# Performance work log

Hardware: AMD Instinct MI355X
Metric: run time of the kernel (lower is better)

## Reference

```python
import jax, jax.numpy as jnp
import numpy as np
from jax import lax

T, B = 128, 256
I, H = 512, 1024
V, O = 128, 64


def setup_inputs() -> dict:
    key = jax.random.key(0)
    ks = jax.random.split(key, 8)
    s_ih = 1.0 / np.sqrt(H)
    return {
        "input": jax.random.randint(ks[0], (T, B), 0, V, dtype=jnp.int64),
        "h0": jnp.zeros((1, B, H), jnp.float32),
        "c0": jnp.zeros((1, B, H), jnp.float32),
        "emb": jax.random.normal(ks[1], (V, I), jnp.float32),
        "w_ih": jax.random.uniform(ks[2], (4 * H, I), jnp.float32, -s_ih, s_ih),
        "w_hh": jax.random.uniform(ks[3], (4 * H, H), jnp.float32, -s_ih, s_ih),
        "b_ih": jax.random.uniform(ks[4], (4 * H,), jnp.float32, -s_ih, s_ih),
        "b_hh": jax.random.uniform(ks[5], (4 * H,), jnp.float32, -s_ih, s_ih),
        "w_out": jax.random.uniform(ks[6], (O, H), jnp.float32, -s_ih, s_ih),
        "b_out": jax.random.uniform(ks[7], (O,), jnp.float32, -s_ih, s_ih),
    }


def reference(input, h0, c0, emb, w_ih, w_hh, b_ih, b_hh, w_out, b_out):
    # Embedding lookup: [T, B] -> [T, B, I]
    x = emb[input]
    b = b_ih + b_hh  # fuse the two bias adds

    def step(carry, xt):
        h, c = carry  # [B, H] each
        gates = xt @ w_ih.T + h @ w_hh.T + b  # [B, 4H]
        i, f, g, o = jnp.split(gates, 4, axis=-1)  # torch gate order: i,f,g,o
        i = jax.nn.sigmoid(i)
        f = jax.nn.sigmoid(f)
        g = jnp.tanh(g)
        o = jax.nn.sigmoid(o)
        c_new = f * c + i * g
        h_new = o * jnp.tanh(c_new)
        return (h_new, c_new), h_new

    (h_last, _), _ = lax.scan(step, (h0[0], c0[0]), x)
    # out_layer(lstm_out[-1].unsqueeze(0))[-1] == last hidden through linear head
    return h_last @ w_out.T + b_out  # [B, O]
```

## Files before the change

kernel.cpp:

```cpp
#include <hip/hip_runtime.h>

typedef __attribute__((ext_vector_type(4)))  int int4v;
typedef __attribute__((ext_vector_type(16))) int i32x16;

union B16 { int4v v; signed char c[16]; };

__device__ __forceinline__ float rcp_(float x){ return __builtin_amdgcn_rcpf(x); }
__device__ __forceinline__ float sigm(float x){ return rcp_(1.f + __expf(-x)); }
__device__ __forceinline__ float tanh_(float x){
  float e = __expf(-2.f * fabsf(x));
  float r = (1.f - e) * rcp_(1.f + e);
  return copysignf(r, x);
}
__device__ __forceinline__ void h_limbs(float h, int& a1, int& a0){
  float f1 = floorf(h * 128.f);
  f1 = fminf(fmaxf(f1, -128.f), 127.f);
  float r = fmaf(h, 32768.f, f1 * -256.f) - 128.f;
  float f0 = fminf(rintf(r), 127.f);
  a1 = (int)f1; a0 = (int)f0;
}

__device__ __forceinline__ void issue_l128_cc(const void* p, int4v& d){
  asm volatile("global_load_dwordx4 %0, %1, off sc0 sc1" : "=&v"(d) : "v"(p) : "memory");
}

__global__ __launch_bounds__(256) void prep_kernel(
    const float* __restrict__ emb, const float* __restrict__ w_ih,
    const float* __restrict__ b_ih, const float* __restrict__ b_hh,
    const float* __restrict__ h0, float* __restrict__ G_in,
    char* __restrict__ a1buf, char* __restrict__ a0buf)
{
  __shared__ __align__(16) float wt[16 * 512];
  const int tid = threadIdx.x;
  const int colbase = blockIdx.x << 4;
  #pragma unroll
  for (int i = 0; i < 8; ++i){
    int f = tid + (i << 8);
    int r = f >> 7, q = (f & 127) << 2;
    *(float4*)&wt[(r << 9) + q] = *(const float4*)&w_ih[((size_t)(colbase + r) << 9) + q];
  }
  __syncthreads();
  const int v_ = tid & 127, ch = tid >> 7;
  float acc[8] = {0,0,0,0,0,0,0,0};
  const float* ep = emb + ((size_t)v_ << 9);
  for (int kq = 0; kq < 128; ++kq){
    float4 e = *(const float4*)(ep + (kq << 2));
    #pragma unroll
    for (int c = 0; c < 8; ++c){
      float4 w = *(const float4*)&wt[(((ch << 3) + c) << 9) + (kq << 2)];
      acc[c] += e.x * w.x + e.y * w.y + e.z * w.z + e.w * w.w;
    }
  }
  const int col0 = colbase + (ch << 3);
  #pragma unroll
  for (int c = 0; c < 8; ++c) acc[c] += b_ih[col0 + c] + b_hh[col0 + c];
  float* gp = &G_in[((size_t)v_ << 12) + col0];
  float4 r0 = {acc[0], acc[1], acc[2], acc[3]};
  float4 r1 = {acc[4], acc[5], acc[6], acc[7]};
  *(float4*)gp = r0;
  *(float4*)(gp + 4) = r1;

  int g0 = (blockIdx.x << 10) + (tid << 2);
  float4 hv = *(const float4*)&h0[g0];
  int a1x,a0x,a1y,a0y,a1z,a0z,a1w,a0w;
  h_limbs(hv.x, a1x, a0x); h_limbs(hv.y, a1y, a0y);
  h_limbs(hv.z, a1z, a0z); h_limbs(hv.w, a1w, a0w);
  unsigned u1 = (unsigned)(a1x & 255) | ((unsigned)(a1y & 255) << 8)
              | ((unsigned)(a1z & 255) << 16) | ((unsigned)(a1w & 255) << 24);
  unsigned u0 = (unsigned)(a0x & 255) | ((unsigned)(a0y & 255) << 8)
              | ((unsigned)(a0z & 255) << 16) | ((unsigned)(a0w & 255) << 24);
  ((unsigned*)a1buf)[g0 >> 2] = u1;
  ((unsigned*)a0buf)[g0 >> 2] = u0;
}

__global__ __launch_bounds__(256, 1) void lstm_kernel(
    const int* __restrict__ input, const float* __restrict__ c0,
    const float* __restrict__ w_hh, const float* __restrict__ w_out,
    const float* __restrict__ b_out, const float* __restrict__ G_in,
    char* __restrict__ a1base, char* __restrict__ a0base,
    unsigned* __restrict__ flags, float* __restrict__ out)
{
  const int tid  = threadIdx.x;
  const int lane = tid & 63;
  const int wid  = tid >> 6;
  const int bg   = blockIdx.x >> 5;
  const int cg   = blockIdx.x & 31;
  const int bl   = tid >> 3;
  const int u4   = (tid & 7) << 2;
  const int row  = tid & 31;
  const int grp  = tid >> 5;

  __shared__ __align__(16) unsigned long long sA1[4096];
  __shared__ __align__(16) unsigned long long sA0[4096];
  __shared__ __align__(16) float sG[32 * 132];
  __shared__ float sKc[128];

  int4v b1f[32], b0f[32];
  {
    const float* wrow = w_hh + (size_t)(wid * 1024 + cg * 32 + (lane & 31)) * 1024;
    const int kb0 = (lane >> 5) << 4;
    float csum = 0.f;
    #pragma unroll
    for (int ks = 0; ks < 32; ++ks){
      B16 v1, v0;
      #pragma unroll
      for (int q = 0; q < 4; ++q){
        float4 w4 = *(const float4*)&wrow[ks * 32 + kb0 + (q << 2)];
        float wa[4] = {w4.x, w4.y, w4.z, w4.w};
        #pragma unroll
        for (int j = 0; j < 4; ++j){
          float w = wa[j];
          csum += w;
          float s1 = rintf(w * 2048.f);
          float s0 = fminf(rintf(fmaf(w, 524288.f, s1 * -256.f)), 127.f);
          v1.c[(q << 2) + j] = (signed char)(int)s1;
          v0.c[(q << 2) + j] = (signed char)(int)s0;
        }
      }
      b1f[ks] = v1.v; b0f[ks] = v0.v;
    }
    csum += __shfl_xor(csum, 32, 64);
    if (lane < 32) sKc[(wid << 5) + lane] = csum * 0.00390625f;
  }

  const int b = (bg << 5) + bl;
  float4 cr = *(const float4*)&c0[((size_t)b << 10) + (cg << 5) + u4];
  unsigned* slots = &flags[bg * 32];
  unsigned* myslot = &flags[bg * 32 + cg];
  const size_t rbase = (size_t)((bg << 5) + row) << 10;

  #pragma unroll 1
  for (int t = 0; t < 128; ++t){
    const char* s1b = a1base + (size_t)(t & 1) * 262144;
    const char* s0b = a0base + (size_t)(t & 1) * 262144;
    char* d1b = a1base + (size_t)((t + 1) & 1) * 262144;
    char* d0b = a0base + (size_t)((t + 1) & 1) * 262144;
    const unsigned target = (unsigned)t;

    int iv = input[t * 256 + b];
    const float* gp = G_in + ((size_t)iv << 12) + (cg << 5) + u4;
    float4 q0 = *(const float4*)(gp);
    float4 q1 = *(const float4*)(gp + 1024);
    float4 q2 = *(const float4*)(gp + 2048);
    float4 q3 = *(const float4*)(gp + 3072);

    if (wid == 0 && target){
      int guard = 0;
      for (;;){
        unsigned v = (lane < 32)
          ? __hip_atomic_load(&slots[lane], __ATOMIC_RELAXED, __HIP_MEMORY_SCOPE_AGENT)
          : 0xFFFFFFFFu;
        if (__ballot(lane >= 16 || v >= target) == ~0ull) break;
        if (++guard > (1 << 20)) break;
      }
    }
    __syncthreads();

    int4v gv1[8], gv0[8];
    #pragma unroll
    for (int i = 0; i < 4; ++i){
      size_t off = rbase + ((size_t)(grp + (i << 3)) << 4);
      issue_l128_cc(s1b + off, gv1[i]);
      issue_l128_cc(s0b + off, gv0[i]);
    }

    if (wid == 0 && target){
      int guard = 0;
      for (;;){
        unsigned v = (lane < 32)
          ? __hip_atomic_load(&slots[lane], __ATOMIC_RELAXED, __HIP_MEMORY_SCOPE_AGENT)
          : 0xFFFFFFFFu;
        if (__ballot(v >= target) == ~0ull) break;
        if (++guard > (1 << 20)) break;
      }
    }
    __syncthreads();

    #pragma unroll
    for (int i = 4; i < 8; ++i){
      size_t off = rbase + ((size_t)(grp + (i << 3)) << 4);
      issue_l128_cc(s1b + off, gv1[i]);
      issue_l128_cc(s0b + off, gv0[i]);
    }

    i32x16 acc_hi = {}, acc_m1 = {}, acc_m2 = {};
    const int4v* A1 = (const int4v*)sA1;
    const int4v* A0 = (const int4v*)sA0;
    #pragma unroll
    for (int c = 0; c < 4; ++c){
      if      (c == 0) asm volatile("s_waitcnt vmcnt(12)" ::: "memory");
      else if (c == 1) asm volatile("s_waitcnt vmcnt(8)"  ::: "memory");
      else if (c == 2) asm volatile("s_waitcnt vmcnt(4)"  ::: "memory");
      else             asm volatile("s_waitcnt vmcnt(0)"  ::: "memory");
      __builtin_amdgcn_sched_barrier(0);
      #pragma unroll
      for (int j = 0; j < 2; ++j){
        const int i = 2*c + j;
        const int m = grp + (i << 3);
        const int lidx = ((((m >> 1) << 6) + ((m & 1) << 5) + row)) << 1;
        *(int4v*)&sA1[lidx] = gv1[i];
        *(int4v*)&sA0[lidx] = gv0[i];
      }
      asm volatile("s_waitcnt lgkmcnt(0)" ::: "memory");
      __builtin_amdgcn_sched_barrier(0);
      __builtin_amdgcn_s_barrier();
      __builtin_amdgcn_sched_barrier(0);
      #pragma unroll
      for (int ks = 8*c; ks < 8*c + 8; ++ks){
        int4v af1 = A1[(ks << 6) + lane];
        acc_hi = __builtin_amdgcn_mfma_i32_32x32x32_i8(af1, b1f[ks], acc_hi, 0, 0, 0);
        acc_m1 = __builtin_amdgcn_mfma_i32_32x32x32_i8(af1, b0f[ks], acc_m1, 0, 0, 0);
        int4v af0 = A0[(ks << 6) + lane];
        acc_m2 = __builtin_amdgcn_mfma_i32_32x32x32_i8(af0, b1f[ks], acc_m2, 0, 0, 0);
      }
    }

    {
      const int col = (wid << 5) + (lane & 31);
      const int rb  = (lane >> 5) << 2;
      #pragma unroll
      for (int r = 0; r < 16; ++r){
        int rrow = (r & 3) + ((r >> 2) << 3) + rb;
        sG[rrow * 132 + col] = 3.814697265625e-06f     * (float)acc_hi[r]
                             + 1.4901161193847656e-08f * (float)(acc_m1[r] + acc_m2[r]);
      }
    }
    __syncthreads();

    {
      float4 kI = *(const float4*)&sKc[ 0 + u4];
      float4 kF = *(const float4*)&sKc[32 + u4];
      float4 kG = *(const float4*)&sKc[64 + u4];
      float4 kO = *(const float4*)&sKc[96 + u4];
      float4 gI = *(const float4*)&sG[bl * 132 +  0 + u4];
      float4 gF = *(const float4*)&sG[bl * 132 + 32 + u4];
      float4 gG = *(const float4*)&sG[bl * 132 + 64 + u4];
      float4 gO = *(const float4*)&sG[bl * 132 + 96 + u4];
      int a1x,a0x,a1y,a0y,a1z,a0z,a1w,a0w;
      { float I=sigm(gI.x+q0.x+kI.x), F=sigm(gF.x+q1.x+kF.x), G=tanh_(gG.x+q2.x+kG.x), O=sigm(gO.x+q3.x+kO.x);
        float Cn=F*cr.x+I*G; cr.x=Cn; h_limbs(O*tanh_(Cn), a1x, a0x); }
      { float I=sigm(gI.y+q0.y+kI.y), F=sigm(gF.y+q1.y+kF.y), G=tanh_(gG.y+q2.y+kG.y), O=sigm(gO.y+q3.y+kO.y);
        float Cn=F*cr.y+I*G; cr.y=Cn; h_limbs(O*tanh_(Cn), a1y, a0y); }
      { float I=sigm(gI.z+q0.z+kI.z), F=sigm(gF.z+q1.z+kF.z), G=tanh_(gG.z+q2.z+kG.z), O=sigm(gO.z+q3.z+kO.z);
        float Cn=F*cr.z+I*G; cr.z=Cn; h_limbs(O*tanh_(Cn), a1z, a0z); }
      { float I=sigm(gI.w+q0.w+kI.w), F=sigm(gF.w+q1.w+kF.w), G=tanh_(gG.w+q2.w+kG.w), O=sigm(gO.w+q3.w+kO.w);
        float Cn=F*cr.w+I*G; cr.w=Cn; h_limbs(O*tanh_(Cn), a1w, a0w); }
      unsigned u1 = (unsigned)(a1x & 255) | ((unsigned)(a1y & 255) << 8)
                  | ((unsigned)(a1z & 255) << 16) | ((unsigned)(a1w & 255) << 24);
      unsigned u0 = (unsigned)(a0x & 255) | ((unsigned)(a0y & 255) << 8)
                  | ((unsigned)(a0z & 255) << 16) | ((unsigned)(a0w & 255) << 24);
      size_t eidx = (((size_t)b << 10) + (cg << 5) + u4) >> 2;
      __hip_atomic_store((unsigned*)d1b + eidx, u1, __ATOMIC_RELAXED, __HIP_MEMORY_SCOPE_AGENT);
      __hip_atomic_store((unsigned*)d0b + eidx, u0, __ATOMIC_RELAXED, __HIP_MEMORY_SCOPE_AGENT);
    }
    __syncthreads();
    if (tid == 0)
      __hip_atomic_store(myslot, (unsigned)(t + 1), __ATOMIC_RELAXED, __HIP_MEMORY_SCOPE_AGENT);
  }

  if (wid == 0){
    int guard = 0;
    for (;;){
      unsigned v = (lane < 32)
        ? __hip_atomic_load(&slots[lane], __ATOMIC_RELAXED, __HIP_MEMORY_SCOPE_AGENT)
        : 0xFFFFFFFFu;
      if (__ballot(v >= 128u) == ~0ull) break;
      if (++guard > (1 << 20)) break;
    }
  }
  __syncthreads();
  {
    const unsigned* h1p = (const unsigned*)a1base;
    const unsigned* h0p = (const unsigned*)a0base;
    const int ksl = tid & 7;
    const int o0 = cg << 1;
    float s0 = 0.f, s1 = 0.f;
    const float* w0p = w_out + ((size_t)o0 << 10);
    const float* w1p = w0p + 1024;
    for (int k = ksl * 128; k < ksl * 128 + 128; k += 4){
      size_t idx = (((size_t)b << 10) + k) >> 2;
      unsigned v1 = __hip_atomic_load(h1p + idx, __ATOMIC_RELAXED, __HIP_MEMORY_SCOPE_AGENT);
      unsigned v0 = __hip_atomic_load(h0p + idx, __ATOMIC_RELAXED, __HIP_MEMORY_SCOPE_AGENT);
      float4 w0 = *(const float4*)(w0p + k);
      float4 w1 = *(const float4*)(w1p + k);
      float hh[4];
      #pragma unroll
      for (int j = 0; j < 4; ++j){
        int A1j = (int)(signed char)((v1 >> (8 * j)) & 255);
        int A0j = (int)(signed char)((v0 >> (8 * j)) & 255);
        hh[j] = (float)(A1j * 256 + A0j + 128) * 3.0517578125e-05f;
      }
      s0 += hh[0]*w0.x + hh[1]*w0.y + hh[2]*w0.z + hh[3]*w0.w;
      s1 += hh[0]*w1.x + hh[1]*w1.y + hh[2]*w1.z + hh[3]*w1.w;
    }
    sG[bl * 16 + (ksl << 1)]     = s0;
    sG[bl * 16 + (ksl << 1) + 1] = s1;
  }
  __syncthreads();
  if (tid < 64){
    int bl2 = tid >> 1, ol = tid & 1;
    float s = b_out[(cg << 1) + ol];
    #pragma unroll
    for (int q = 0; q < 8; ++q) s += sG[bl2 * 16 + (q << 1) + ol];
    out[((size_t)((bg << 5) + bl2) << 6) + (cg << 1) + ol] = s;
  }
}

extern "C" void kernel_launch(void* const* d_in, const int* in_sizes, int n_in,
                              void* d_out, int out_size, void* d_ws, size_t ws_size,
                              hipStream_t stream){
  (void)in_sizes; (void)n_in; (void)out_size; (void)ws_size;
  const int* input   = (const int*)d_in[0];
  const float* h0    = (const float*)d_in[1];
  const float* c0    = (const float*)d_in[2];
  const float* emb   = (const float*)d_in[3];
  const float* w_ih  = (const float*)d_in[4];
  const float* w_hh  = (const float*)d_in[5];
  const float* b_ih  = (const float*)d_in[6];
  const float* b_hh  = (const float*)d_in[7];
  const float* w_out = (const float*)d_in[8];
  const float* b_out = (const float*)d_in[9];
  float* out = (float*)d_out;

  char* ws = (char*)d_ws;
  float* G_in   = (float*)ws;
  char* a1buf   = ws + (2u << 20);
  char* a0buf   = ws + (2u << 20) + (512u << 10);
  unsigned* flags = (unsigned*)(ws + (3u << 20));

  hipMemsetAsync(flags, 0, 4096, stream);
  prep_kernel<<<dim3(256), dim3(256), 0, stream>>>(emb, w_ih, b_ih, b_hh, h0, G_in, a1buf, a0buf);

  void* args[] = {(void*)&input, (void*)&c0, (void*)&w_hh, (void*)&w_out, (void*)&b_out,
                  (void*)&G_in, (void*)&a1buf, (void*)&a0buf, (void*)&flags, (void*)&out};
  if (hipLaunchCooperativeKernel((void*)lstm_kernel, dim3(256), dim3(256), args, 0, stream)
      != hipSuccess){
    lstm_kernel<<<dim3(256), dim3(256), 0, stream>>>(input, c0, w_hh, w_out, b_out,
                                                     G_in, a1buf, a0buf, flags, out);
  }
}
```

Baseline: 1.004 ms.

## Split recurrent K-dimension across two wave halves with 512-thread blocks

Doubles the block to 512 threads so each gate has two waves, each holding half of the K slices of the quantized recurrent weights in registers. Each half runs the MFMAs only for its K chunks and writes partial gates to separate shared buffers, which the first 256 threads sum before the elementwise update. The goal is to halve the serial MFMA chain per wave on each timestep's critical path and to cut register pressure. The cost is extra shared memory, an added partial-sum reduction, and idle waves during the elementwise and output phases.

Result: faster. 943.9 us (-6.0%).

```diff
diff --git a/kernel.cpp b/kernel.cpp
--- a/kernel.cpp
+++ b/kernel.cpp
@@ -73,7 +73,7 @@
   ((unsigned*)a0buf)[g0 >> 2] = u0;
 }
 
-__global__ __launch_bounds__(256, 1) void lstm_kernel(
+__global__ __launch_bounds__(512, 1) void lstm_kernel(
     const int* __restrict__ input, const float* __restrict__ c0,
     const float* __restrict__ w_hh, const float* __restrict__ w_out,
     const float* __restrict__ b_out, const float* __restrict__ G_in,
@@ -83,29 +83,31 @@
   const int tid  = threadIdx.x;
   const int lane = tid & 63;
   const int wid  = tid >> 6;
+  const int gate = wid & 3;
+  const int half = wid >> 2;
   const int bg   = blockIdx.x >> 5;
   const int cg   = blockIdx.x & 31;
-  const int bl   = tid >> 3;
-  const int u4   = (tid & 7) << 2;
   const int row  = tid & 31;
   const int grp  = tid >> 5;
 
   __shared__ __align__(16) unsigned long long sA1[4096];
   __shared__ __align__(16) unsigned long long sA0[4096];
-  __shared__ __align__(16) float sG[32 * 132];
-  __shared__ float sKc[128];
-
-  int4v b1f[32], b0f[32];
+  __shared__ __align__(16) float sGa[32 * 132];
+  __shared__ __align__(16) float sGb[32 * 132];
+  __shared__ float sKc2[2][128];
+
+  int4v b1f[16], b0f[16];
   {
-    const float* wrow = w_hh + (size_t)(wid * 1024 + cg * 32 + (lane & 31)) * 1024;
+    const float* wrow = w_hh + (size_t)(gate * 1024 + cg * 32 + (lane & 31)) * 1024;
     const int kb0 = (lane >> 5) << 4;
     float csum = 0.f;
     #pragma unroll
-    for (int ks = 0; ks < 32; ++ks){
+    for (int ksl = 0; ksl < 16; ++ksl){
+      const int gks = (ksl & 7) + ((ksl >> 3) << 4) + (half << 3);
       B16 v1, v0;
       #pragma unroll
       for (int q = 0; q < 4; ++q){
-        float4 w4 = *(const float4*)&wrow[ks * 32 + kb0 + (q << 2)];
+        float4 w4 = *(const float4*)&wrow[gks * 32 + kb0 + (q << 2)];
         float wa[4] = {w4.x, w4.y, w4.z, w4.w};
         #pragma unroll
         for (int j = 0; j < 4; ++j){
@@ -117,14 +119,17 @@
           v0.c[(q << 2) + j] = (signed char)(int)s0;
         }
       }
-      b1f[ks] = v1.v; b0f[ks] = v0.v;
+      b1f[ksl] = v1.v; b0f[ksl] = v0.v;
     }
     csum += __shfl_xor(csum, 32, 64);
-    if (lane < 32) sKc[(wid << 5) + lane] = csum * 0.00390625f;
-  }
-
-  const int b = (bg << 5) + bl;
-  float4 cr = *(const float4*)&c0[((size_t)b << 10) + (cg << 5) + u4];
+    if (lane < 32) sKc2[half][(gate << 5) + lane] = csum * 0.00390625f;
+  }
+
+  const int bl = (tid >> 3) & 31;
+  const int u4 = (tid & 7) << 2;
+  const int b  = (bg << 5) + bl;
+  float4 cr = {0,0,0,0};
+  if (tid < 256) cr = *(const float4*)&c0[((size_t)b << 10) + (cg << 5) + u4];
   unsigned* slots = &flags[bg * 32];
   unsigned* myslot = &flags[bg * 32 + cg];
   const size_t rbase = (size_t)((bg << 5) + row) << 10;
@@ -137,12 +142,15 @@
     char* d0b = a0base + (size_t)((t + 1) & 1) * 262144;
     const unsigned target = (unsigned)t;
 
-    int iv = input[t * 256 + b];
-    const float* gp = G_in + ((size_t)iv << 12) + (cg << 5) + u4;
-    float4 q0 = *(const float4*)(gp);
-    float4 q1 = *(const float4*)(gp + 1024);
-    float4 q2 = *(const float4*)(gp + 2048);
-    float4 q3 = *(const float4*)(gp + 3072);
+    float4 q0 = {0,0,0,0}, q1 = {0,0,0,0}, q2 = {0,0,0,0}, q3 = {0,0,0,0};
+    if (tid < 256){
+      int iv = input[t * 256 + b];
+      const float* gp = G_in + ((size_t)iv << 12) + (cg << 5) + u4;
+      q0 = *(const float4*)(gp);
+      q1 = *(const float4*)(gp + 1024);
+      q2 = *(const float4*)(gp + 2048);
+      q3 = *(const float4*)(gp + 3072);
+    }
 
     if (wid == 0 && target){
       int guard = 0;
@@ -156,10 +164,10 @@
     }
     __syncthreads();
 
-    int4v gv1[8], gv0[8];
-    #pragma unroll
-    for (int i = 0; i < 4; ++i){
-      size_t off = rbase + ((size_t)(grp + (i << 3)) << 4);
+    int4v gv1[4], gv0[4];
+    #pragma unroll
+    for (int i = 0; i < 2; ++i){
+      size_t off = rbase + ((size_t)(grp + (i << 4)) << 4);
       issue_l128_cc(s1b + off, gv1[i]);
       issue_l128_cc(s0b + off, gv0[i]);
     }
@@ -177,8 +185,8 @@
     __syncthreads();
 
     #pragma unroll
-    for (int i = 4; i < 8; ++i){
-      size_t off = rbase + ((size_t)(grp + (i << 3)) << 4);
+    for (int i = 2; i < 4; ++i){
+      size_t off = rbase + ((size_t)(grp + (i << 4)) << 4);
       issue_l128_cc(s1b + off, gv1[i]);
       issue_l128_cc(s0b + off, gv0[i]);
     }
@@ -188,54 +196,66 @@
     const int4v* A0 = (const int4v*)sA0;
     #pragma unroll
     for (int c = 0; c < 4; ++c){
-      if      (c == 0) asm volatile("s_waitcnt vmcnt(12)" ::: "memory");
-      else if (c == 1) asm volatile("s_waitcnt vmcnt(8)"  ::: "memory");
-      else if (c == 2) asm volatile("s_waitcnt vmcnt(4)"  ::: "memory");
-      else             asm volatile("s_waitcnt vmcnt(0)"  ::: "memory");
+      if      (c == 0) asm volatile("s_waitcnt vmcnt(6)" ::: "memory");
+      else if (c == 1) asm volatile("s_waitcnt vmcnt(4)" ::: "memory");
+      else if (c == 2) asm volatile("s_waitcnt vmcnt(2)" ::: "memory");
+      else             asm volatile("s_waitcnt vmcnt(0)" ::: "memory");
       __builtin_amdgcn_sched_barrier(0);
-      #pragma unroll
-      for (int j = 0; j < 2; ++j){
-        const int i = 2*c + j;
-        const int m = grp + (i << 3);
+      {
+        const int m = grp + (c << 4);
         const int lidx = ((((m >> 1) << 6) + ((m & 1) << 5) + row)) << 1;
-        *(int4v*)&sA1[lidx] = gv1[i];
-        *(int4v*)&sA0[lidx] = gv0[i];
+        *(int4v*)&sA1[lidx] = gv1[c];
+        *(int4v*)&sA0[lidx] = gv0[c];
       }
       asm volatile("s_waitcnt lgkmcnt(0)" ::: "memory");
       __builtin_amdgcn_sched_barrier(0);
       __builtin_amdgcn_s_barrier();
       __builtin_amdgcn_sched_barrier(0);
-      #pragma unroll
-      for (int ks = 8*c; ks < 8*c + 8; ++ks){
-        int4v af1 = A1[(ks << 6) + lane];
-        acc_hi = __builtin_amdgcn_mfma_i32_32x32x32_i8(af1, b1f[ks], acc_hi, 0, 0, 0);
-        acc_m1 = __builtin_amdgcn_mfma_i32_32x32x32_i8(af1, b0f[ks], acc_m1, 0, 0, 0);
-        int4v af0 = A0[(ks << 6) + lane];
-        acc_m2 = __builtin_amdgcn_mfma_i32_32x32x32_i8(af0, b1f[ks], acc_m2, 0, 0, 0);
+      if (half == (c & 1)){
+        const int ksl0 = (c >> 1) << 3;
+        #pragma unroll
+        for (int k8 = 0; k8 < 8; ++k8){
+          const int ks  = (c << 3) + k8;
+          const int ksl = ksl0 + k8;
+          int4v af1 = A1[(ks << 6) + lane];
+          acc_hi = __builtin_amdgcn_mfma_i32_32x32x32_i8(af1, b1f[ksl], acc_hi, 0, 0, 0);
+          acc_m1 = __builtin_amdgcn_mfma_i32_32x32x32_i8(af1, b0f[ksl], acc_m1, 0, 0, 0);
+          int4v af0 = A0[(ks << 6) + lane];
+          acc_m2 = __builtin_amdgcn_mfma_i32_32x32x32_i8(af0, b1f[ksl], acc_m2, 0, 0, 0);
+        }
       }
     }
 
     {
-      const int col = (wid << 5) + (lane & 31);
+      float* sGh = half ? sGb : sGa;
+      const int col = (gate << 5) + (lane & 31);
       const int rb  = (lane >> 5) << 2;
       #pragma unroll
       for (int r = 0; r < 16; ++r){
         int rrow = (r & 3) + ((r >> 2) << 3) + rb;
-        sG[rrow * 132 + col] = 3.814697265625e-06f     * (float)acc_hi[r]
-                             + 1.4901161193847656e-08f * (float)(acc_m1[r] + acc_m2[r]);
+        sGh[rrow * 132 + col] = 3.814697265625e-06f     * (float)acc_hi[r]
+                              + 1.4901161193847656e-08f * (float)(acc_m1[r] + acc_m2[r]);
       }
     }
     __syncthreads();
 
-    {
-      float4 kI = *(const float4*)&sKc[ 0 + u4];
-      float4 kF = *(const float4*)&sKc[32 + u4];
-      float4 kG = *(const float4*)&sKc[64 + u4];
-      float4 kO = *(const float4*)&sKc[96 + u4];
-      float4 gI = *(const float4*)&sG[bl * 132 +  0 + u4];
-      float4 gF = *(const float4*)&sG[bl * 132 + 32 + u4];
-      float4 gG = *(const float4*)&sG[bl * 132 + 64 + u4];
-      float4 gO = *(const float4*)&sG[bl * 132 + 96 + u4];
+    if (tid < 256){
+      float4 kIa = *(const float4*)&sKc2[0][ 0 + u4], kIb = *(const float4*)&sKc2[1][ 0 + u4];
+      float4 kFa = *(const float4*)&sKc2[0][32 + u4], kFb = *(const float4*)&sKc2[1][32 + u4];
+      float4 kGa = *(const float4*)&sKc2[0][64 + u4], kGb = *(const float4*)&sKc2[1][64 + u4];
+      float4 kOa = *(const float4*)&sKc2[0][96 + u4], kOb = *(const float4*)&sKc2[1][96 + u4];
+      float4 gIa = *(const float4*)&sGa[bl * 132 +  0 + u4], gIb = *(const float4*)&sGb[bl * 132 +  0 + u4];
+      float4 gFa = *(const float4*)&sGa[bl * 132 + 32 + u4], gFb = *(const float4*)&sGb[bl * 132 + 32 + u4];
+      float4 gGa = *(const float4*)&sGa[bl * 132 + 64 + u4], gGb = *(const float4*)&sGb[bl * 132 + 64 + u4];
+      float4 gOa = *(const float4*)&sGa[bl * 132 + 96 + u4], gOb = *(const float4*)&sGb[bl * 132 + 96 + u4];
+      float4 gI = {gIa.x+gIb.x, gIa.y+gIb.y, gIa.z+gIb.z, gIa.w+gIb.w};
+      float4 gF = {gFa.x+gFb.x, gFa.y+gFb.y, gFa.z+gFb.z, gFa.w+gFb.w};
+      float4 gG = {gGa.x+gGb.x, gGa.y+gGb.y, gGa.z+gGb.z, gGa.w+gGb.w};
+      float4 gO = {gOa.x+gOb.x, gOa.y+gOb.y, gOa.z+gOb.z, gOa.w+gOb.w};
+      float4 kI = {kIa.x+kIb.x, kIa.y+kIb.y, kIa.z+kIb.z, kIa.w+kIb.w};
+      float4 kF = {kFa.x+kFb.x, kFa.y+kFb.y, kFa.z+kFb.z, kFa.w+kFb.w};
+      float4 kG = {kGa.x+kGb.x, kGa.y+kGb.y, kGa.z+kGb.z, kGa.w+kGb.w};
+      float4 kO = {kOa.x+kOb.x, kOa.y+kOb.y, kOa.z+kOb.z, kOa.w+kOb.w};
       int a1x,a0x,a1y,a0y,a1z,a0z,a1w,a0w;
       { float I=sigm(gI.x+q0.x+kI.x), F=sigm(gF.x+q1.x+kF.x), G=tanh_(gG.x+q2.x+kG.x), O=sigm(gO.x+q3.x+kO.x);
         float Cn=F*cr.x+I*G; cr.x=Cn; h_limbs(O*tanh_(Cn), a1x, a0x); }
@@ -269,7 +289,7 @@
     }
   }
   __syncthreads();
-  {
+  if (tid < 256){
     const unsigned* h1p = (const unsigned*)a1base;
     const unsigned* h0p = (const unsigned*)a0base;
     const int ksl = tid & 7;
@@ -293,15 +313,15 @@
       s0 += hh[0]*w0.x + hh[1]*w0.y + hh[2]*w0.z + hh[3]*w0.w;
       s1 += hh[0]*w1.x + hh[1]*w1.y + hh[2]*w1.z + hh[3]*w1.w;
     }
-    sG[bl * 16 + (ksl << 1)]     = s0;
-    sG[bl * 16 + (ksl << 1) + 1] = s1;
+    sGa[bl * 16 + (ksl << 1)]     = s0;
+    sGa[bl * 16 + (ksl << 1) + 1] = s1;
   }
   __syncthreads();
   if (tid < 64){
     int bl2 = tid >> 1, ol = tid & 1;
     float s = b_out[(cg << 1) + ol];
     #pragma unroll
-    for (int q = 0; q < 8; ++q) s += sG[bl2 * 16 + (q << 1) + ol];
+    for (int q = 0; q < 8; ++q) s += sGa[bl2 * 16 + (q << 1) + ol];
     out[((size_t)((bg << 5) + bl2) << 6) + (cg << 1) + ol] = s;
   }
 }
@@ -333,9 +353,9 @@
 
   void* args[] = {(void*)&input, (void*)&c0, (void*)&w_hh, (void*)&w_out, (void*)&b_out,
                   (void*)&G_in, (void*)&a1buf, (void*)&a0buf, (void*)&flags, (void*)&out};
-  if (hipLaunchCooperativeKernel((void*)lstm_kernel, dim3(256), dim3(256), args, 0, stream)
+  if (hipLaunchCooperativeKernel((void*)lstm_kernel, dim3(256), dim3(512), args, 0, stream)
       != hipSuccess){
-    lstm_kernel<<<dim3(256), dim3(256), 0, stream>>>(input, c0, w_hh, w_out, b_out,
+    lstm_kernel<<<dim3(256), dim3(512), 0, stream>>>(input, c0, w_hh, w_out, b_out,
                                                      G_in, a1buf, a0buf, flags, out);
   }
 }
```
